# Kernel optimization log

Measured on AMD Instinct MI355X. Metric: run time of the kernel, lower is better.

## Reference

```python
import jax, jax.numpy as jnp
import numpy as np

B, DIM, H, W = 4, 128, 128, 128
NH, DH = 8, 16               # num_heads, dim_head = dim // num_heads
GH_HI, GH_LO = 4, 4          # group_split = [4, 4]
WIN = 8                      # window_size for low-freq avgpool
SCALE = DH ** -0.5


def conv1x1(x, w, b):
    # x: (b,c,h,w), w: (o,c), b: (o,)
    return jnp.einsum('bchw,oc->bohw', x, w) + b[None, :, None, None]


def dwconv3(x, w, b):
    # depthwise 3x3, w: (C,1,3,3) OIHW with feature_group_count=C
    y = jax.lax.conv_general_dilated(x, w, (1, 1), 'SAME',
                                     feature_group_count=x.shape[1],
                                     dimension_numbers=('NCHW', 'OIHW', 'NCHW'))
    return y + b[None, :, None, None]


def setup_inputs() -> dict:
    key = jax.random.key(0)
    ks = jax.random.split(key, 10)
    def rn(k, shape, s=0.05):
        return jax.random.normal(k, shape, jnp.float32) * s
    C3 = 3 * GH_HI * DH            # 192: qkv channels for high-freq branch
    CH = GH_HI * DH                # 64:  high-freq value channels
    CL = GH_LO * DH                # 64:  low-freq q channels
    return {
        'x': jax.random.normal(ks[0], (B, DIM, H, W), jnp.float32),
        'Wqkv': rn(ks[1], (C3, DIM)), 'bqkv': jnp.zeros((C3,), jnp.float32),
        'Wdw': rn(ks[2], (C3, 1, 3, 3)), 'bdw': jnp.zeros((C3,), jnp.float32),
        'Wa1': rn(ks[3], (CH, CH)), 'ba1': jnp.zeros((CH,), jnp.float32),
        'Wa2': rn(ks[4], (CH, CH)), 'ba2': jnp.zeros((CH,), jnp.float32),
        'Wq': rn(ks[5], (CL, DIM)), 'bq': jnp.zeros((CL,), jnp.float32),
        'Wkv': rn(ks[6], (2 * CL, DIM)), 'bkv': jnp.zeros((2 * CL,), jnp.float32),
        'Wproj': rn(ks[7], (DIM, DIM)), 'bproj': jnp.zeros((DIM,), jnp.float32),
    }


def reference(x, Wqkv, bqkv, Wdw, bdw, Wa1, ba1, Wa2, ba2, Wq, bq, Wkv, bkv, Wproj, bproj):
    b = x.shape[0]
    # ---- high-frequency branch: conv qkv -> depthwise mix -> AttnMap(q*k) -> tanh gate * v
    qkv = dwconv3(conv1x1(x, Wqkv, bqkv), Wdw, bdw)          # (b, 3*64, h, w)
    q, k, v = jnp.split(qkv, 3, axis=1)                      # each (b, 64, h, w)
    a = conv1x1(q * k, Wa1, ba1)
    a = a * jax.nn.sigmoid(a)                                # MemoryEfficientSwish
    a = conv1x1(a, Wa2, ba2)
    res_h = jnp.tanh(a * SCALE) * v                          # (b, 64, h, w)
    # ---- low-frequency branch: full-res Q vs avgpooled KV softmax attention
    qg = conv1x1(x, Wq, bq).reshape(b, GH_LO, DH, H * W).transpose(0, 1, 3, 2)  # (b,h,hw,d)
    xp = x.reshape(b, DIM, H // WIN, WIN, W // WIN, WIN).mean((3, 5))           # avgpool 8x8
    hw_p = (H // WIN) * (W // WIN)
    kv = conv1x1(xp, Wkv, bkv).reshape(b, 2, GH_LO, DH, hw_p).transpose(1, 0, 2, 4, 3)
    k2, v2 = kv[0], kv[1]                                     # (b, heads, hw_p, d)
    attn = jax.nn.softmax(SCALE * jnp.einsum('bhnd,bhmd->bhnm', qg, k2), axis=-1)
    res_l = jnp.einsum('bhnm,bhmd->bhnd', attn, v2)           # (b, heads, hw, d)
    res_l = res_l.transpose(0, 1, 3, 2).reshape(b, GH_LO * DH, H, W)
    # ---- concat branches and project
    return conv1x1(jnp.concatenate([res_h, res_l], axis=1), Wproj, bproj)
```

## Files before the change

kernel.cpp:

```cpp
#include <hip/hip_runtime.h>
#include <hip/hip_bf16.h>

typedef __hip_bfloat16 bf16;
typedef short short8v __attribute__((ext_vector_type(8)));
typedef short short4v __attribute__((ext_vector_type(4)));
typedef float floatx4 __attribute__((ext_vector_type(4)));

#define HW 16384

__device__ __forceinline__ float b2f(bf16 v) { return __bfloat162float(v); }
__device__ __forceinline__ bf16 f2b(float v) { return __float2bfloat16(v); }
__device__ __forceinline__ short f2bs(float v) { bf16 h = __float2bfloat16(v); return __builtin_bit_cast(short, h); }
__device__ __forceinline__ float bs2f(short s) { return b2f(__builtin_bit_cast(bf16, s)); }
__device__ __forceinline__ int wuniform(int v) { return __builtin_amdgcn_readfirstlane(v); }

#define OFFB_XP    0u
#define OFFB_K2    524288u
#define OFFB_V2    786432u
#define OFFB_QKVG  (1u << 20)
#define OFFB_RESH  (33u << 20)

__global__ __launch_bounds__(256) void k_pool(const float* __restrict__ x, float* __restrict__ xp,
                                              const float* __restrict__ Wqkv, const float* __restrict__ Wq,
                                              short* __restrict__ wconv)
{
    int idx = blockIdx.x * 256 + threadIdx.x;
    int j = idx & 15, i = (idx >> 4) & 15, bc = idx >> 8;
    const float* src = x + (size_t)bc * HW + (i * 8) * 128 + j * 8;
    float s = 0.f;
    #pragma unroll
    for (int u = 0; u < 8; u++) {
        #pragma unroll
        for (int t = 0; t < 8; t++) s += src[u * 128 + t];
    }
    xp[bc * 256 + i * 16 + j] = s * (1.f / 64.f);

    if (blockIdx.x < 8) {
        int base = blockIdx.x * 4096 + threadIdx.x * 16;
        #pragma unroll
        for (int e = 0; e < 16; e += 4) {
            int k = base + e;
            const float* ws = (k < 24576) ? (Wqkv + k) : (Wq + k - 24576);
            floatx4 wv = *(const floatx4*)ws;
            short4v pk;
            pk[0] = f2bs(wv[0]); pk[1] = f2bs(wv[1]); pk[2] = f2bs(wv[2]); pk[3] = f2bs(wv[3]);
            *(short4v*)&wconv[k] = pk;
        }
    }
}

__global__ __launch_bounds__(256) void k_kv(const float* __restrict__ xp,
                                            const float* __restrict__ Wkv, const float* __restrict__ bkv,
                                            float* __restrict__ k2, float* __restrict__ v2)
{
    __shared__ float w_s[128];
    int o = blockIdx.x & 127, b = blockIdx.x >> 7;
    int m = threadIdx.x;
    if (m < 128) w_s[m] = Wkv[o * 128 + m];
    __syncthreads();
    const float* xb = xp + b * 32768 + m;
    float s0 = 0.f, s1 = 0.f, s2 = 0.f, s3 = 0.f;
    #pragma unroll
    for (int c = 0; c < 128; c += 4) {
        s0 += w_s[c]     * xb[(size_t)(c)     * 256];
        s1 += w_s[c + 1] * xb[(size_t)(c + 1) * 256];
        s2 += w_s[c + 2] * xb[(size_t)(c + 2) * 256];
        s3 += w_s[c + 3] * xb[(size_t)(c + 3) * 256];
    }
    float a = bkv[o] + ((s0 + s1) + (s2 + s3));
    int sb = o >> 6, r = o & 63, gh = r >> 4, dh = r & 15;
    float* dst = sb == 0 ? k2 : v2;
    dst[((b * 4 + gh) * 256 + m) * 16 + dh] = a;
}

__global__ __launch_bounds__(256) void k_conv(const float* __restrict__ x,
                                              const short* __restrict__ wconv,
                                              const float* __restrict__ bqkv, const float* __restrict__ bq,
                                              bf16* __restrict__ qkvg)
{
    __shared__ short a_s[128 * 128];
    __shared__ short b_s[128 * 128];
    __shared__ float bias_s[256];
    int t = threadIdx.x;
    int b = blockIdx.y;
    int px0 = blockIdx.x * 128;

    bias_s[t] = (t < 192) ? bqkv[t] : bq[t - 192];

    int wave = wuniform(t >> 6);
    int lane = t & 63;
    int quad = lane >> 4, l16 = lane & 15;
    int pxs = t & 127, chalf = (t >> 7) * 64;

    {
        const float* xb = x + (size_t)b * 128 * HW + px0 + pxs;
        #pragma unroll
        for (int p = 0; p < 8; p++) {
            int c0 = chalf + p * 8;
            float xv[8];
            #pragma unroll
            for (int jj = 0; jj < 8; jj++) xv[jj] = xb[(size_t)(c0 + jj) * HW];
            short8v pk;
            #pragma unroll
            for (int jj = 0; jj < 8; jj++) pk[jj] = f2bs(xv[jj]);
            *(short8v*)&b_s[((c0 >> 3) * 128 + pxs) * 8] = pk;
        }
    }

    #pragma unroll 1
    for (int my = 0; my < 2; my++) {
        __syncthreads();
        const short* wsrc = wconv + my * 16384;
        #pragma unroll
        for (int i = 0; i < 8; i++) {
            int idx = i * 2048 + t * 8;
            *(short8v*)&a_s[idx] = *(const short8v*)&wsrc[idx];
        }
        __syncthreads();

        floatx4 acc[2][8] = {};
        #pragma unroll
        for (int kk = 0; kk < 4; kk++) {
            short8v a0 = *(const short8v*)&a_s[(wave * 32 + l16) * 128 + kk * 32 + quad * 8];
            short8v a1 = *(const short8v*)&a_s[(wave * 32 + 16 + l16) * 128 + kk * 32 + quad * 8];
            #pragma unroll
            for (int nt = 0; nt < 8; nt++) {
                short8v bv = *(const short8v*)&b_s[((kk * 4 + quad) * 128 + nt * 16 + l16) * 8];
                acc[0][nt] = __builtin_amdgcn_mfma_f32_16x16x32_bf16(a0, bv, acc[0][nt], 0, 0, 0);
                acc[1][nt] = __builtin_amdgcn_mfma_f32_16x16x32_bf16(a1, bv, acc[1][nt], 0, 0, 0);
            }
        }
        #pragma unroll
        for (int m = 0; m < 2; m++) {
            int rowb = wave * 32 + m * 16 + quad * 4;
            #pragma unroll
            for (int nt = 0; nt < 8; nt++) {
                int px = px0 + nt * 16 + l16;
                #pragma unroll
                for (int r = 0; r < 4; r++) {
                    int row = rowb + r;
                    float val = acc[m][nt][r] + bias_s[my * 128 + row];
                    qkvg[((size_t)b * 256 + my * 128 + row) * HW + px] = f2b(val);
                }
            }
        }
    }
}

__global__ __launch_bounds__(256) void k_dw(const bf16* __restrict__ qkvg,
                                            const float* __restrict__ Wdw, const float* __restrict__ bdw,
                                            bf16* __restrict__ p, bf16* __restrict__ v)
{
    int blk = blockIdx.x;
    int bc = blk >> 3;
    int c = bc & 63, b = bc >> 6;
    int g = (blk & 7) * 256 + threadIdx.x;
    int i = g >> 4;
    int j0 = (g & 15) * 8;
    float acc[3][8];
    #pragma unroll
    for (int pl = 0; pl < 3; pl++) {
        float bias = bdw[pl * 64 + c];
        #pragma unroll
        for (int t2 = 0; t2 < 8; t2++) acc[pl][t2] = bias;
    }
    #pragma unroll
    for (int pl = 0; pl < 3; pl++) {
        const bf16* plane = qkvg + (size_t)(b * 256 + pl * 64 + c) * HW;
        const float* w = Wdw + (pl * 64 + c) * 9;
        #pragma unroll
        for (int dy = 0; dy < 3; dy++) {
            int ii = i + dy - 1;
            float e[10];
            if ((unsigned)ii < 128u) {
                const bf16* r = plane + ii * 128 + j0;
                short8v v8 = *(const short8v*)r;
                #pragma unroll
                for (int t2 = 0; t2 < 8; t2++) e[t2 + 1] = bs2f(v8[t2]);
                e[0] = (j0 > 0) ? b2f(r[-1]) : 0.f;
                e[9] = (j0 < 120) ? b2f(r[8]) : 0.f;
            } else {
                #pragma unroll
                for (int t2 = 0; t2 < 10; t2++) e[t2] = 0.f;
            }
            float wa = w[dy * 3], wb = w[dy * 3 + 1], wc = w[dy * 3 + 2];
            #pragma unroll
            for (int t2 = 0; t2 < 8; t2++)
                acc[pl][t2] += wa * e[t2] + wb * e[t2 + 1] + wc * e[t2 + 2];
        }
    }
    short8v pv, vv;
    #pragma unroll
    for (int t2 = 0; t2 < 8; t2++) {
        pv[t2] = f2bs(acc[0][t2] * acc[1][t2]);
        vv[t2] = f2bs(acc[2][t2]);
    }
    size_t off = (size_t)(b * 64 + c) * HW + i * 128 + j0;
    *(short8v*)(p + off) = pv;
    *(short8v*)(v + off) = vv;
}

__global__ __launch_bounds__(256, 6) void k_attn(bf16* __restrict__ qkvg, const float* __restrict__ k2,
                                                 const float* __restrict__ v2)
{
    __shared__ short kt[16 * 64 * 8];
    __shared__ short vt[8 * 64 * 8];
    int t = threadIdx.x;
    int h = blockIdx.y, b = blockIdx.z;
    int px0b = blockIdx.x * 64;
    const float* K = k2 + (size_t)(b * 4 + h) * 4096;
    const float* V = v2 + (size_t)(b * 4 + h) * 4096;
    bf16* Qbase = qkvg + (size_t)(b * 256 + 192 + h * 16) * HW + px0b;

    {
        int mb = t >> 5, kl = t & 31, q = kl >> 3, s = kl & 7;
        int tile = 2 * mb + (s >> 2), row = q * 4 + (s & 3);
        float4 k0 = *(const float4*)(K + t * 16);
        float4 k1 = *(const float4*)(K + t * 16 + 4);
        float4 kx2 = *(const float4*)(K + t * 16 + 8);
        float4 k3 = *(const float4*)(K + t * 16 + 12);
        short8v lo, hi, zz = {};
        lo[0] = f2bs(k0.x); lo[1] = f2bs(k0.y); lo[2] = f2bs(k0.z); lo[3] = f2bs(k0.w);
        lo[4] = f2bs(k1.x); lo[5] = f2bs(k1.y); lo[6] = f2bs(k1.z); lo[7] = f2bs(k1.w);
        hi[0] = f2bs(kx2.x); hi[1] = f2bs(kx2.y); hi[2] = f2bs(kx2.z); hi[3] = f2bs(kx2.w);
        hi[4] = f2bs(k3.x); hi[5] = f2bs(k3.y); hi[6] = f2bs(k3.z); hi[7] = f2bs(k3.w);
        *(short8v*)&kt[(tile * 64 + row) * 8] = lo;
        *(short8v*)&kt[(tile * 64 + 16 + row) * 8] = hi;
        *(short8v*)&kt[(tile * 64 + 32 + row) * 8] = zz;
        *(short8v*)&kt[(tile * 64 + 48 + row) * 8] = zz;
    }
    #pragma unroll
    for (int u = 0; u < 2; u++) {
        int f = t * 2 + u;
        int mb = f >> 6, lane = f & 63, quad = lane >> 4, d = lane & 15;
        short8v pk;
        #pragma unroll
        for (int i = 0; i < 8; i++) pk[i] = f2bs(V[(mb * 32 + quad * 8 + i) * 16 + d]);
        *(short8v*)&vt[f * 8] = pk;
    }

    int wave = wuniform(t >> 6);
    int lane = t & 63;
    int quad = lane >> 4, l16 = lane & 15;
    short8v qf = {};
    if (quad < 2) {
        int px = wave * 16 + l16;
        #pragma unroll
        for (int i = 0; i < 8; i++)
            qf[i] = f2bs(b2f(Qbase[(size_t)(quad * 8 + i) * HW + px]) * 0.36067376022224085f);
    }
    __syncthreads();

    {
        int pxt = wave;
        floatx4 denv = {};
        floatx4 oa = {};
        #pragma unroll
        for (int mb = 0; mb < 8; mb++) {
            short8v kfE = *(const short8v*)&kt[((2 * mb) * 64 + lane) * 8];
            short8v kfO = *(const short8v*)&kt[((2 * mb + 1) * 64 + lane) * 8];
            floatx4 scE = __builtin_amdgcn_mfma_f32_16x16x32_bf16(kfE, qf, (floatx4){0.f, 0.f, 0.f, 0.f}, 0, 0, 0);
            floatx4 scO = __builtin_amdgcn_mfma_f32_16x16x32_bf16(kfO, qf, (floatx4){0.f, 0.f, 0.f, 0.f}, 0, 0, 0);
            floatx4 peE, peO;
            #pragma unroll
            for (int r = 0; r < 4; r++) {
                peE[r] = exp2f(fminf(scE[r], 86.f));
                peO[r] = exp2f(fminf(scO[r], 86.f));
            }
            denv += peE;
            denv += peO;
            short8v pa;
            pa[0] = f2bs(peE[0]); pa[1] = f2bs(peE[1]); pa[2] = f2bs(peE[2]); pa[3] = f2bs(peE[3]);
            pa[4] = f2bs(peO[0]); pa[5] = f2bs(peO[1]); pa[6] = f2bs(peO[2]); pa[7] = f2bs(peO[3]);
            short8v vf = *(const short8v*)&vt[(mb * 64 + lane) * 8];
            oa = __builtin_amdgcn_mfma_f32_16x16x32_bf16(vf, pa, oa, 0, 0, 0);
        }
        float den = (denv[0] + denv[1]) + (denv[2] + denv[3]);
        den += __shfl_xor(den, 16, 64);
        den += __shfl_xor(den, 32, 64);
        float rden = 1.f / den;
        #pragma unroll
        for (int r = 0; r < 4; r++)
            Qbase[(size_t)(quad * 4 + r) * HW + pxt * 16 + l16] = f2b(oa[r] * rden);
    }
}

__global__ __launch_bounds__(256) void k_wcvt(const float* __restrict__ Wproj,
                                              const float* __restrict__ Wa1, const float* __restrict__ Wa2,
                                              short* __restrict__ wdst)
{
    int idx = blockIdx.x * 1024 + threadIdx.x * 4;
    const float* src;
    if (idx < 16384)      src = Wproj + idx;
    else if (idx < 20480) src = Wa1 + (idx - 16384);
    else                  src = Wa2 + (idx - 20480);
    floatx4 wv = *(const floatx4*)src;
    short4v pk;
    pk[0] = f2bs(wv[0]); pk[1] = f2bs(wv[1]); pk[2] = f2bs(wv[2]); pk[3] = f2bs(wv[3]);
    *(short4v*)&wdst[idx] = pk;
}

__global__ __launch_bounds__(256) void k_resh(const bf16* __restrict__ p, const bf16* __restrict__ vhat,
                                              const short* __restrict__ wabf,
                                              const float* __restrict__ ba1, const float* __restrict__ ba2,
                                              bf16* __restrict__ resh)
{
    __shared__ short aw1[64 * 64];
    __shared__ short aw2[64 * 64];
    __shared__ short bp[8 * 128 * 8];
    __shared__ short bs2[8 * 128 * 8];
    __shared__ float b1s[64], b2s[64];
    int t = threadIdx.x;
    int b = blockIdx.y;
    int px0 = blockIdx.x * 128;

    if (t < 64) { b1s[t] = ba1[t]; b2s[t] = ba2[t]; }
    #pragma unroll
    for (int i = 0; i < 2; i++) {
        int idx = i * 2048 + t * 8;
        *(short8v*)&aw1[idx] = *(const short8v*)&wabf[idx];
        *(short8v*)&aw2[idx] = *(const short8v*)&wabf[4096 + idx];
    }
    {
        int pxs = t & 127, chalf = (t >> 7) * 32;
        const short* pb = (const short*)p + (size_t)b * 64 * HW + px0 + pxs;
        #pragma unroll
        for (int pp = 0; pp < 4; pp++) {
            int c0 = chalf + pp * 8;
            short8v pk;
            #pragma unroll
            for (int jj = 0; jj < 8; jj++) pk[jj] = pb[(size_t)(c0 + jj) * HW];
            *(short8v*)&bp[((c0 >> 3) * 128 + pxs) * 8] = pk;
        }
    }
    __syncthreads();

    int wave = wuniform(t >> 6);
    int lane = t & 63;
    int quad = lane >> 4, l16 = lane & 15;
    int k0 = wave * 16 + quad * 4;

    floatx4 acc1[8] = {};
    #pragma unroll
    for (int kk = 0; kk < 2; kk++) {
        short8v af = *(const short8v*)&aw1[(wave * 16 + l16) * 64 + kk * 32 + quad * 8];
        #pragma unroll
        for (int nt = 0; nt < 8; nt++) {
            short8v bf = *(const short8v*)&bp[((kk * 4 + quad) * 128 + nt * 16 + l16) * 8];
            acc1[nt] = __builtin_amdgcn_mfma_f32_16x16x32_bf16(af, bf, acc1[nt], 0, 0, 0);
        }
    }
    #pragma unroll
    for (int nt = 0; nt < 8; nt++) {
        int px = nt * 16 + l16;
        short4v pk;
        #pragma unroll
        for (int r = 0; r < 4; r++) {
            float a = acc1[nt][r] + b1s[k0 + r];
            pk[r] = f2bs(a / (1.f + __expf(-a)));
        }
        *(short4v*)&bs2[((k0 >> 3) * 128 + px) * 8 + (k0 & 7)] = pk;
    }
    __syncthreads();

    floatx4 acc2[8] = {};
    #pragma unroll
    for (int kk = 0; kk < 2; kk++) {
        short8v af = *(const short8v*)&aw2[(wave * 16 + l16) * 64 + kk * 32 + quad * 8];
        #pragma unroll
        for (int nt = 0; nt < 8; nt++) {
            short8v bf = *(const short8v*)&bs2[((kk * 4 + quad) * 128 + nt * 16 + l16) * 8];
            acc2[nt] = __builtin_amdgcn_mfma_f32_16x16x32_bf16(af, bf, acc2[nt], 0, 0, 0);
        }
    }
    #pragma unroll
    for (int nt = 0; nt < 8; nt++) {
        int px = px0 + nt * 16 + l16;
        #pragma unroll
        for (int r = 0; r < 4; r++) {
            int oc = k0 + r;
            float g = tanhf((acc2[nt][r] + b2s[oc]) * 0.25f);
            float vv = b2f(vhat[(size_t)(b * 64 + oc) * HW + px]);
            resh[(size_t)(b * 64 + oc) * HW + px] = f2b(g * vv);
        }
    }
}

__global__ __launch_bounds__(256) void k_proj(const bf16* __restrict__ resh, const bf16* __restrict__ qkvg,
                                              const short* __restrict__ wpbf, const float* __restrict__ bproj,
                                              float* __restrict__ out)
{
    __shared__ short a_s[128 * 128];
    __shared__ short b_s[128 * 128];
    __shared__ float bias_s[128];
    int t = threadIdx.x;
    int b = blockIdx.y;
    int px0 = blockIdx.x * 128;
    const bf16* resl = qkvg + (size_t)(b * 256 + 192) * HW;

    if (t < 128) bias_s[t] = bproj[t];
    #pragma unroll
    for (int i = 0; i < 8; i++) {
        int idx = i * 2048 + t * 8;
        *(short8v*)&a_s[idx] = *(const short8v*)&wpbf[idx];
    }
    {
        int pxs = t & 127, half = t >> 7;
        const short* srcb = half == 0 ? ((const short*)resh + (size_t)b * 64 * HW + px0 + pxs)
                                      : ((const short*)resl + px0 + pxs);
        #pragma unroll
        for (int pp = 0; pp < 8; pp++) {
            int c0 = half * 64 + pp * 8;
            short8v pk;
            #pragma unroll
            for (int jj = 0; jj < 8; jj++) pk[jj] = srcb[(size_t)(pp * 8 + jj) * HW];
            *(short8v*)&b_s[((c0 >> 3) * 128 + pxs) * 8] = pk;
        }
    }
    __syncthreads();

    int wave = wuniform(t >> 6);
    int lane = t & 63;
    int quad = lane >> 4, l16 = lane & 15;
    floatx4 acc[2][8] = {};
    #pragma unroll
    for (int kk = 0; kk < 4; kk++) {
        short8v a0 = *(const short8v*)&a_s[(wave * 32 + l16) * 128 + kk * 32 + quad * 8];
        short8v a1 = *(const short8v*)&a_s[(wave * 32 + 16 + l16) * 128 + kk * 32 + quad * 8];
        #pragma unroll
        for (int nt = 0; nt < 8; nt++) {
            short8v bv = *(const short8v*)&b_s[((kk * 4 + quad) * 128 + nt * 16 + l16) * 8];
            acc[0][nt] = __builtin_amdgcn_mfma_f32_16x16x32_bf16(a0, bv, acc[0][nt], 0, 0, 0);
            acc[1][nt] = __builtin_amdgcn_mfma_f32_16x16x32_bf16(a1, bv, acc[1][nt], 0, 0, 0);
        }
    }
    #pragma unroll
    for (int m = 0; m < 2; m++) {
        int rowb = wave * 32 + m * 16 + quad * 4;
        #pragma unroll
        for (int nt = 0; nt < 8; nt++) {
            int px = px0 + nt * 16 + l16;
            #pragma unroll
            for (int r = 0; r < 4; r++) {
                int row = rowb + r;
                out[((size_t)b * 128 + row) * HW + px] = acc[m][nt][r] + bias_s[row];
            }
        }
    }
}

extern "C" void kernel_launch(void* const* d_in, const int* in_sizes, int n_in,
                              void* d_out, int out_size, void* d_ws, size_t ws_size,
                              hipStream_t stream)
{
    (void)in_sizes; (void)n_in; (void)out_size; (void)ws_size;
    const float* x     = (const float*)d_in[0];
    const float* Wqkv  = (const float*)d_in[1];
    const float* bqkv  = (const float*)d_in[2];
    const float* Wdw   = (const float*)d_in[3];
    const float* bdw   = (const float*)d_in[4];
    const float* Wa1   = (const float*)d_in[5];
    const float* ba1   = (const float*)d_in[6];
    const float* Wa2   = (const float*)d_in[7];
    const float* ba2   = (const float*)d_in[8];
    const float* Wq    = (const float*)d_in[9];
    const float* bq    = (const float*)d_in[10];
    const float* Wkv   = (const float*)d_in[11];
    const float* bkv   = (const float*)d_in[12];
    const float* Wproj = (const float*)d_in[13];
    const float* bproj = (const float*)d_in[14];

    char* wsb = (char*)d_ws;
    float* xp   = (float*)(wsb + OFFB_XP);
    float* k2   = (float*)(wsb + OFFB_K2);
    float* v2   = (float*)(wsb + OFFB_V2);
    bf16*  qkvg = (bf16*)(wsb + OFFB_QKVG);
    bf16*  resh = (bf16*)(wsb + OFFB_RESH);
    short* wconv = (short*)(wsb + OFFB_RESH);
    short* wlate = (short*)(wsb + OFFB_K2);
    bf16*  p    = (bf16*)d_out;
    bf16*  v    = (bf16*)d_out + 4194304;
    float* out  = (float*)d_out;

    k_pool<<<dim3(512), 256, 0, stream>>>(x, xp, Wqkv, Wq, wconv);
    k_kv<<<dim3(512), 256, 0, stream>>>(xp, Wkv, bkv, k2, v2);
    k_conv<<<dim3(128, 4), 256, 0, stream>>>(x, wconv, bqkv, bq, qkvg);
    k_dw<<<dim3(2048), 256, 0, stream>>>(qkvg, Wdw, bdw, p, v);
    k_attn<<<dim3(256, 4, 4), 256, 0, stream>>>(qkvg, k2, v2);
    k_wcvt<<<dim3(24), 256, 0, stream>>>(Wproj, Wa1, Wa2, wlate);
    k_resh<<<dim3(128, 4), 256, 0, stream>>>(p, v, wlate + 16384, ba1, ba2, resh);
    k_proj<<<dim3(128, 4), 256, 0, stream>>>(resh, qkvg, wlate, bproj, out);
}
```

Before: 200.9 us.

## Merge independent kernels into combined launches via block-index branching

Cuts the launch count from eight to four by packing independent stages into one grid each: pointwise QKV conv with avgpool, KV projection with depthwise conv, and low-frequency attention with the high-frequency gating MLP. Block ID picks which stage a block runs. Weight conversion to bf16, previously done by separate kernels, now happens inside each consumer block. The goal is to remove launch gaps and let small stages overlap with large ones, at the cost of repeating the weight conversion in every block and sizing shared memory for the larger branch.

```diff
diff --git a/kernel.cpp b/kernel.cpp
--- a/kernel.cpp
+++ b/kernel.cpp
@@ -20,374 +20,363 @@
 #define OFFB_QKVG  (1u << 20)
 #define OFFB_RESH  (33u << 20)
 
-__global__ __launch_bounds__(256) void k_pool(const float* __restrict__ x, float* __restrict__ xp,
-                                              const float* __restrict__ Wqkv, const float* __restrict__ Wq,
-                                              short* __restrict__ wconv)
+__global__ __launch_bounds__(256) void k_fuseA(const float* __restrict__ x,
+                                               const float* __restrict__ Wqkv, const float* __restrict__ bqkv,
+                                               const float* __restrict__ Wq,  const float* __restrict__ bq,
+                                               bf16* __restrict__ qkvg, float* __restrict__ xp)
 {
-    int idx = blockIdx.x * 256 + threadIdx.x;
-    int j = idx & 15, i = (idx >> 4) & 15, bc = idx >> 8;
-    const float* src = x + (size_t)bc * HW + (i * 8) * 128 + j * 8;
-    float s = 0.f;
-    #pragma unroll
-    for (int u = 0; u < 8; u++) {
-        #pragma unroll
-        for (int t = 0; t < 8; t++) s += src[u * 128 + t];
-    }
-    xp[bc * 256 + i * 16 + j] = s * (1.f / 64.f);
-
-    if (blockIdx.x < 8) {
-        int base = blockIdx.x * 4096 + threadIdx.x * 16;
-        #pragma unroll
-        for (int e = 0; e < 16; e += 4) {
-            int k = base + e;
-            const float* ws = (k < 24576) ? (Wqkv + k) : (Wq + k - 24576);
-            floatx4 wv = *(const floatx4*)ws;
-            short4v pk;
-            pk[0] = f2bs(wv[0]); pk[1] = f2bs(wv[1]); pk[2] = f2bs(wv[2]); pk[3] = f2bs(wv[3]);
-            *(short4v*)&wconv[k] = pk;
-        }
+    __shared__ __align__(16) char smem[66560];
+    int t = threadIdx.x;
+    int bid = blockIdx.x;
+
+    if (bid < 512) {
+        short* a_s = (short*)smem;
+        short* b_s = (short*)(smem + 32768);
+        float* bias_s = (float*)(smem + 65536);
+        int b = bid >> 7;
+        int px0 = (bid & 127) * 128;
+
+        bias_s[t] = (t < 192) ? bqkv[t] : bq[t - 192];
+
+        int wave = wuniform(t >> 6);
+        int lane = t & 63;
+        int quad = lane >> 4, l16 = lane & 15;
+        int pxs = t & 127, chalf = (t >> 7) * 64;
+
+        {
+            const float* xb = x + (size_t)b * 128 * HW + px0 + pxs;
+            #pragma unroll
+            for (int p = 0; p < 8; p++) {
+                int c0 = chalf + p * 8;
+                float xv[8];
+                #pragma unroll
+                for (int jj = 0; jj < 8; jj++) xv[jj] = xb[(size_t)(c0 + jj) * HW];
+                short8v pk;
+                #pragma unroll
+                for (int jj = 0; jj < 8; jj++) pk[jj] = f2bs(xv[jj]);
+                *(short8v*)&b_s[((c0 >> 3) * 128 + pxs) * 8] = pk;
+            }
+        }
+
+        #pragma unroll 1
+        for (int my = 0; my < 2; my++) {
+            __syncthreads();
+            #pragma unroll
+            for (int i = 0; i < 16; i++) {
+                int idx = i * 1024 + t * 4;
+                int row = idx >> 7, col = idx & 127;
+                int oc = my * 128 + row;
+                const float* srcw = (oc < 192) ? (Wqkv + oc * 128 + col) : (Wq + (oc - 192) * 128 + col);
+                floatx4 wv = *(const floatx4*)srcw;
+                short4v pk4;
+                pk4[0] = f2bs(wv[0]); pk4[1] = f2bs(wv[1]); pk4[2] = f2bs(wv[2]); pk4[3] = f2bs(wv[3]);
+                *(short4v*)&a_s[row * 128 + col] = pk4;
+            }
+            __syncthreads();
+
+            floatx4 acc[2][8] = {};
+            #pragma unroll
+            for (int kk = 0; kk < 4; kk++) {
+                short8v a0 = *(const short8v*)&a_s[(wave * 32 + l16) * 128 + kk * 32 + quad * 8];
+                short8v a1 = *(const short8v*)&a_s[(wave * 32 + 16 + l16) * 128 + kk * 32 + quad * 8];
+                #pragma unroll
+                for (int nt = 0; nt < 8; nt++) {
+                    short8v bv = *(const short8v*)&b_s[((kk * 4 + quad) * 128 + nt * 16 + l16) * 8];
+                    acc[0][nt] = __builtin_amdgcn_mfma_f32_16x16x32_bf16(a0, bv, acc[0][nt], 0, 0, 0);
+                    acc[1][nt] = __builtin_amdgcn_mfma_f32_16x16x32_bf16(a1, bv, acc[1][nt], 0, 0, 0);
+                }
+            }
+            #pragma unroll
+            for (int m = 0; m < 2; m++) {
+                int rowb = wave * 32 + m * 16 + quad * 4;
+                #pragma unroll
+                for (int nt = 0; nt < 8; nt++) {
+                    int px = px0 + nt * 16 + l16;
+                    #pragma unroll
+                    for (int r = 0; r < 4; r++) {
+                        int row = rowb + r;
+                        float val = acc[m][nt][r] + bias_s[my * 128 + row];
+                        qkvg[((size_t)b * 256 + my * 128 + row) * HW + px] = f2b(val);
+                    }
+                }
+            }
+        }
+    } else {
+        int idx = (bid - 512) * 256 + t;
+        int j = idx & 15, i = (idx >> 4) & 15, bc = idx >> 8;
+        const float* src = x + (size_t)bc * HW + (i * 8) * 128 + j * 8;
+        float s = 0.f;
+        #pragma unroll
+        for (int u = 0; u < 8; u++) {
+            #pragma unroll
+            for (int t2 = 0; t2 < 8; t2++) s += src[u * 128 + t2];
+        }
+        xp[bc * 256 + i * 16 + j] = s * (1.f / 64.f);
     }
 }
 
-__global__ __launch_bounds__(256) void k_kv(const float* __restrict__ xp,
-                                            const float* __restrict__ Wkv, const float* __restrict__ bkv,
-                                            float* __restrict__ k2, float* __restrict__ v2)
+__global__ __launch_bounds__(256) void k_fuseB(const float* __restrict__ xp,
+                                               const float* __restrict__ Wkv, const float* __restrict__ bkv,
+                                               float* __restrict__ k2, float* __restrict__ v2,
+                                               const bf16* __restrict__ qkvg,
+                                               const float* __restrict__ Wdw, const float* __restrict__ bdw,
+                                               bf16* __restrict__ p, bf16* __restrict__ v)
 {
     __shared__ float w_s[128];
-    int o = blockIdx.x & 127, b = blockIdx.x >> 7;
-    int m = threadIdx.x;
-    if (m < 128) w_s[m] = Wkv[o * 128 + m];
-    __syncthreads();
-    const float* xb = xp + b * 32768 + m;
-    float s0 = 0.f, s1 = 0.f, s2 = 0.f, s3 = 0.f;
-    #pragma unroll
-    for (int c = 0; c < 128; c += 4) {
-        s0 += w_s[c]     * xb[(size_t)(c)     * 256];
-        s1 += w_s[c + 1] * xb[(size_t)(c + 1) * 256];
-        s2 += w_s[c + 2] * xb[(size_t)(c + 2) * 256];
-        s3 += w_s[c + 3] * xb[(size_t)(c + 3) * 256];
-    }
-    float a = bkv[o] + ((s0 + s1) + (s2 + s3));
-    int sb = o >> 6, r = o & 63, gh = r >> 4, dh = r & 15;
-    float* dst = sb == 0 ? k2 : v2;
-    dst[((b * 4 + gh) * 256 + m) * 16 + dh] = a;
+    int t = threadIdx.x;
+    int bid = blockIdx.x;
+
+    if (bid < 512) {
+        int o = bid & 127, b = bid >> 7;
+        int m = t;
+        if (m < 128) w_s[m] = Wkv[o * 128 + m];
+        __syncthreads();
+        const float* xb = xp + b * 32768 + m;
+        float s0 = 0.f, s1 = 0.f, s2 = 0.f, s3 = 0.f;
+        #pragma unroll
+        for (int c = 0; c < 128; c += 4) {
+            s0 += w_s[c]     * xb[(size_t)(c)     * 256];
+            s1 += w_s[c + 1] * xb[(size_t)(c + 1) * 256];
+            s2 += w_s[c + 2] * xb[(size_t)(c + 2) * 256];
+            s3 += w_s[c + 3] * xb[(size_t)(c + 3) * 256];
+        }
+        float a = bkv[o] + ((s0 + s1) + (s2 + s3));
+        int sb = o >> 6, r = o & 63, gh = r >> 4, dh = r & 15;
+        float* dst = sb == 0 ? k2 : v2;
+        dst[((b * 4 + gh) * 256 + m) * 16 + dh] = a;
+    } else {
+        int blk = bid - 512;
+        int bc = blk >> 3;
+        int c = bc & 63, b = bc >> 6;
+        int g = (blk & 7) * 256 + t;
+        int i = g >> 4;
+        int j0 = (g & 15) * 8;
+        float acc[3][8];
+        #pragma unroll
+        for (int pl = 0; pl < 3; pl++) {
+            float bias = bdw[pl * 64 + c];
+            #pragma unroll
+            for (int t2 = 0; t2 < 8; t2++) acc[pl][t2] = bias;
+        }
+        #pragma unroll
+        for (int pl = 0; pl < 3; pl++) {
+            const bf16* plane = qkvg + (size_t)(b * 256 + pl * 64 + c) * HW;
+            const float* w = Wdw + (pl * 64 + c) * 9;
+            #pragma unroll
+            for (int dy = 0; dy < 3; dy++) {
+                int ii = i + dy - 1;
+                float e[10];
+                if ((unsigned)ii < 128u) {
+                    const bf16* r = plane + ii * 128 + j0;
+                    short8v v8 = *(const short8v*)r;
+                    #pragma unroll
+                    for (int t2 = 0; t2 < 8; t2++) e[t2 + 1] = bs2f(v8[t2]);
+                    e[0] = (j0 > 0) ? b2f(r[-1]) : 0.f;
+                    e[9] = (j0 < 120) ? b2f(r[8]) : 0.f;
+                } else {
+                    #pragma unroll
+                    for (int t2 = 0; t2 < 10; t2++) e[t2] = 0.f;
+                }
+                float wa = w[dy * 3], wb = w[dy * 3 + 1], wc = w[dy * 3 + 2];
+                #pragma unroll
+                for (int t2 = 0; t2 < 8; t2++)
+                    acc[pl][t2] += wa * e[t2] + wb * e[t2 + 1] + wc * e[t2 + 2];
+            }
+        }
+        short8v pv, vv;
+        #pragma unroll
+        for (int t2 = 0; t2 < 8; t2++) {
+            pv[t2] = f2bs(acc[0][t2] * acc[1][t2]);
+            vv[t2] = f2bs(acc[2][t2]);
+        }
+        size_t off = (size_t)(b * 64 + c) * HW + i * 128 + j0;
+        *(short8v*)(p + off) = pv;
+        *(short8v*)(v + off) = vv;
+    }
 }
 
-__global__ __launch_bounds__(256) void k_conv(const float* __restrict__ x,
-                                              const short* __restrict__ wconv,
-                                              const float* __restrict__ bqkv, const float* __restrict__ bq,
-                                              bf16* __restrict__ qkvg)
+__global__ __launch_bounds__(256) void k_fuseC(bf16* __restrict__ qkvg,
+                                               const float* __restrict__ k2, const float* __restrict__ v2,
+                                               const bf16* __restrict__ p, const bf16* __restrict__ vhat,
+                                               const float* __restrict__ Wa1, const float* __restrict__ ba1,
+                                               const float* __restrict__ Wa2, const float* __restrict__ ba2,
+                                               bf16* __restrict__ resh)
 {
-    __shared__ short a_s[128 * 128];
-    __shared__ short b_s[128 * 128];
-    __shared__ float bias_s[256];
+    __shared__ __align__(16) char smem[49664];
     int t = threadIdx.x;
-    int b = blockIdx.y;
-    int px0 = blockIdx.x * 128;
-
-    bias_s[t] = (t < 192) ? bqkv[t] : bq[t - 192];
-
-    int wave = wuniform(t >> 6);
-    int lane = t & 63;
-    int quad = lane >> 4, l16 = lane & 15;
-    int pxs = t & 127, chalf = (t >> 7) * 64;
-
-    {
-        const float* xb = x + (size_t)b * 128 * HW + px0 + pxs;
-        #pragma unroll
-        for (int p = 0; p < 8; p++) {
-            int c0 = chalf + p * 8;
-            float xv[8];
-            #pragma unroll
-            for (int jj = 0; jj < 8; jj++) xv[jj] = xb[(size_t)(c0 + jj) * HW];
+    int bid = blockIdx.x;
+
+    if (bid < 512) {
+        short* aw1 = (short*)smem;
+        short* aw2 = (short*)(smem + 8192);
+        short* bp  = (short*)(smem + 16384);
+        short* bs2 = (short*)(smem + 32768);
+        float* b1s = (float*)(smem + 49152);
+        float* b2s = (float*)(smem + 49408);
+        int b = bid >> 7;
+        int px0 = (bid & 127) * 128;
+
+        if (t < 64) { b1s[t] = ba1[t]; b2s[t] = ba2[t]; }
+        #pragma unroll
+        for (int i = 0; i < 4; i++) {
+            int idx = i * 1024 + t * 4;
+            floatx4 w1 = *(const floatx4*)(Wa1 + idx);
+            floatx4 w2 = *(const floatx4*)(Wa2 + idx);
+            short4v p1, p2;
+            #pragma unroll
+            for (int e = 0; e < 4; e++) { p1[e] = f2bs(w1[e]); p2[e] = f2bs(w2[e]); }
+            *(short4v*)&aw1[idx] = p1;
+            *(short4v*)&aw2[idx] = p2;
+        }
+        {
+            int pxs = t & 127, chalf = (t >> 7) * 32;
+            const short* pb = (const short*)p + (size_t)b * 64 * HW + px0 + pxs;
+            #pragma unroll
+            for (int pp = 0; pp < 4; pp++) {
+                int c0 = chalf + pp * 8;
+                short8v pk;
+                #pragma unroll
+                for (int jj = 0; jj < 8; jj++) pk[jj] = pb[(size_t)(c0 + jj) * HW];
+                *(short8v*)&bp[((c0 >> 3) * 128 + pxs) * 8] = pk;
+            }
+        }
+        __syncthreads();
+
+        int wave = wuniform(t >> 6);
+        int lane = t & 63;
+        int quad = lane >> 4, l16 = lane & 15;
+        int k0 = wave * 16 + quad * 4;
+
+        floatx4 acc1[8] = {};
+        #pragma unroll
+        for (int kk = 0; kk < 2; kk++) {
+            short8v af = *(const short8v*)&aw1[(wave * 16 + l16) * 64 + kk * 32 + quad * 8];
+            #pragma unroll
+            for (int nt = 0; nt < 8; nt++) {
+                short8v bf = *(const short8v*)&bp[((kk * 4 + quad) * 128 + nt * 16 + l16) * 8];
+                acc1[nt] = __builtin_amdgcn_mfma_f32_16x16x32_bf16(af, bf, acc1[nt], 0, 0, 0);
+            }
+        }
+        #pragma unroll
+        for (int nt = 0; nt < 8; nt++) {
+            int px = nt * 16 + l16;
+            short4v pk;
+            #pragma unroll
+            for (int r = 0; r < 4; r++) {
+                float a = acc1[nt][r] + b1s[k0 + r];
+                pk[r] = f2bs(a / (1.f + __expf(-a)));
+            }
+            *(short4v*)&bs2[((k0 >> 3) * 128 + px) * 8 + (k0 & 7)] = pk;
+        }
+        __syncthreads();
+
+        floatx4 acc2[8] = {};
+        #pragma unroll
+        for (int kk = 0; kk < 2; kk++) {
+            short8v af = *(const short8v*)&aw2[(wave * 16 + l16) * 64 + kk * 32 + quad * 8];
+            #pragma unroll
+            for (int nt = 0; nt < 8; nt++) {
+                short8v bf = *(const short8v*)&bs2[((kk * 4 + quad) * 128 + nt * 16 + l16) * 8];
+                acc2[nt] = __builtin_amdgcn_mfma_f32_16x16x32_bf16(af, bf, acc2[nt], 0, 0, 0);
+            }
+        }
+        #pragma unroll
+        for (int nt = 0; nt < 8; nt++) {
+            int px = px0 + nt * 16 + l16;
+            #pragma unroll
+            for (int r = 0; r < 4; r++) {
+                int oc = k0 + r;
+                float g = tanhf((acc2[nt][r] + b2s[oc]) * 0.25f);
+                float vv = b2f(vhat[(size_t)(b * 64 + oc) * HW + px]);
+                resh[(size_t)(b * 64 + oc) * HW + px] = f2b(g * vv);
+            }
+        }
+    } else {
+        short* kt = (short*)smem;
+        short* vt = (short*)(smem + 16384);
+        int abid = bid - 512;
+        int h = (abid >> 8) & 3, b = abid >> 10;
+        int px0b = (abid & 255) * 64;
+        const float* K = k2 + (size_t)(b * 4 + h) * 4096;
+        const float* V = v2 + (size_t)(b * 4 + h) * 4096;
+        bf16* Qbase = qkvg + (size_t)(b * 256 + 192 + h * 16) * HW + px0b;
+
+        {
+            int mb = t >> 5, kl = t & 31, q = kl >> 3, s = kl & 7;
+            int tile = 2 * mb + (s >> 2), row = q * 4 + (s & 3);
+            float4 k0 = *(const float4*)(K + t * 16);
+            float4 k1 = *(const float4*)(K + t * 16 + 4);
+            float4 kx2 = *(const float4*)(K + t * 16 + 8);
+            float4 k3 = *(const float4*)(K + t * 16 + 12);
+            short8v lo, hi, zz = {};
+            lo[0] = f2bs(k0.x); lo[1] = f2bs(k0.y); lo[2] = f2bs(k0.z); lo[3] = f2bs(k0.w);
+            lo[4] = f2bs(k1.x); lo[5] = f2bs(k1.y); lo[6] = f2bs(k1.z); lo[7] = f2bs(k1.w);
+            hi[0] = f2bs(kx2.x); hi[1] = f2bs(kx2.y); hi[2] = f2bs(kx2.z); hi[3] = f2bs(kx2.w);
+            hi[4] = f2bs(k3.x); hi[5] = f2bs(k3.y); hi[6] = f2bs(k3.z); hi[7] = f2bs(k3.w);
+            *(short8v*)&kt[(tile * 64 + row) * 8] = lo;
+            *(short8v*)&kt[(tile * 64 + 16 + row) * 8] = hi;
+            *(short8v*)&kt[(tile * 64 + 32 + row) * 8] = zz;
+            *(short8v*)&kt[(tile * 64 + 48 + row) * 8] = zz;
+        }
+        #pragma unroll
+        for (int u = 0; u < 2; u++) {
+            int f = t * 2 + u;
+            int mb = f >> 6, lane = f & 63, quad = lane >> 4, d = lane & 15;
             short8v pk;
             #pragma unroll
-            for (int jj = 0; jj < 8; jj++) pk[jj] = f2bs(xv[jj]);
-            *(short8v*)&b_s[((c0 >> 3) * 128 + pxs) * 8] = pk;
-        }
-    }
-
-    #pragma unroll 1
-    for (int my = 0; my < 2; my++) {
+            for (int i = 0; i < 8; i++) pk[i] = f2bs(V[(mb * 32 + quad * 8 + i) * 16 + d]);
+            *(short8v*)&vt[f * 8] = pk;
+        }
+
+        int wave = wuniform(t >> 6);
+        int lane = t & 63;
+        int quad = lane >> 4, l16 = lane & 15;
+        short8v qf = {};
+        if (quad < 2) {
+            int px = wave * 16 + l16;
+            #pragma unroll
+            for (int i = 0; i < 8; i++)
+                qf[i] = f2bs(b2f(Qbase[(size_t)(quad * 8 + i) * HW + px]) * 0.36067376022224085f);
+        }
         __syncthreads();
-        const short* wsrc = wconv + my * 16384;
-        #pragma unroll
-        for (int i = 0; i < 8; i++) {
-            int idx = i * 2048 + t * 8;
-            *(short8v*)&a_s[idx] = *(const short8v*)&wsrc[idx];
-        }
-        __syncthreads();
-
-        floatx4 acc[2][8] = {};
-        #pragma unroll
-        for (int kk = 0; kk < 4; kk++) {
-            short8v a0 = *(const short8v*)&a_s[(wave * 32 + l16) * 128 + kk * 32 + quad * 8];
-            short8v a1 = *(const short8v*)&a_s[(wave * 32 + 16 + l16) * 128 + kk * 32 + quad * 8];
-            #pragma unroll
-            for (int nt = 0; nt < 8; nt++) {
-                short8v bv = *(const short8v*)&b_s[((kk * 4 + quad) * 128 + nt * 16 + l16) * 8];
-                acc[0][nt] = __builtin_amdgcn_mfma_f32_16x16x32_bf16(a0, bv, acc[0][nt], 0, 0, 0);
-                acc[1][nt] = __builtin_amdgcn_mfma_f32_16x16x32_bf16(a1, bv, acc[1][nt], 0, 0, 0);
-            }
-        }
-        #pragma unroll
-        for (int m = 0; m < 2; m++) {
-            int rowb = wave * 32 + m * 16 + quad * 4;
-            #pragma unroll
-            for (int nt = 0; nt < 8; nt++) {
-                int px = px0 + nt * 16 + l16;
+
+        {
+            int pxt = wave;
+            floatx4 denv = {};
+            floatx4 oa = {};
+            #pragma unroll
+            for (int mb = 0; mb < 8; mb++) {
+                short8v kfE = *(const short8v*)&kt[((2 * mb) * 64 + lane) * 8];
+                short8v kfO = *(const short8v*)&kt[((2 * mb + 1) * 64 + lane) * 8];
+                floatx4 scE = __builtin_amdgcn_mfma_f32_16x16x32_bf16(kfE, qf, (floatx4){0.f, 0.f, 0.f, 0.f}, 0, 0, 0);
+                floatx4 scO = __builtin_amdgcn_mfma_f32_16x16x32_bf16(kfO, qf, (floatx4){0.f, 0.f, 0.f, 0.f}, 0, 0, 0);
+                floatx4 peE, peO;
                 #pragma unroll
                 for (int r = 0; r < 4; r++) {
-                    int row = rowb + r;
-                    float val = acc[m][nt][r] + bias_s[my * 128 + row];
-                    qkvg[((size_t)b * 256 + my * 128 + row) * HW + px] = f2b(val);
+                    peE[r] = exp2f(fminf(scE[r], 86.f));
+                    peO[r] = exp2f(fminf(scO[r], 86.f));
                 }
-            }
+                denv += peE;
+                denv += peO;
+                short8v pa;
+                pa[0] = f2bs(peE[0]); pa[1] = f2bs(peE[1]); pa[2] = f2bs(peE[2]); pa[3] = f2bs(peE[3]);
+                pa[4] = f2bs(peO[0]); pa[5] = f2bs(peO[1]); pa[6] = f2bs(peO[2]); pa[7] = f2bs(peO[3]);
+                short8v vf = *(const short8v*)&vt[(mb * 64 + lane) * 8];
+                oa = __builtin_amdgcn_mfma_f32_16x16x32_bf16(vf, pa, oa, 0, 0, 0);
+            }
+            float den = (denv[0] + denv[1]) + (denv[2] + denv[3]);
+            den += __shfl_xor(den, 16, 64);
+            den += __shfl_xor(den, 32, 64);
+            float rden = 1.f / den;
+            #pragma unroll
+            for (int r = 0; r < 4; r++)
+                Qbase[(size_t)(quad * 4 + r) * HW + pxt * 16 + l16] = f2b(oa[r] * rden);
         }
     }
 }
 
-__global__ __launch_bounds__(256) void k_dw(const bf16* __restrict__ qkvg,
-                                            const float* __restrict__ Wdw, const float* __restrict__ bdw,
-                                            bf16* __restrict__ p, bf16* __restrict__ v)
-{
-    int blk = blockIdx.x;
-    int bc = blk >> 3;
-    int c = bc & 63, b = bc >> 6;
-    int g = (blk & 7) * 256 + threadIdx.x;
-    int i = g >> 4;
-    int j0 = (g & 15) * 8;
-    float acc[3][8];
-    #pragma unroll
-    for (int pl = 0; pl < 3; pl++) {
-        float bias = bdw[pl * 64 + c];
-        #pragma unroll
-        for (int t2 = 0; t2 < 8; t2++) acc[pl][t2] = bias;
-    }
-    #pragma unroll
-    for (int pl = 0; pl < 3; pl++) {
-        const bf16* plane = qkvg + (size_t)(b * 256 + pl * 64 + c) * HW;
-        const float* w = Wdw + (pl * 64 + c) * 9;
-        #pragma unroll
-        for (int dy = 0; dy < 3; dy++) {
-            int ii = i + dy - 1;
-            float e[10];
-            if ((unsigned)ii < 128u) {
-                const bf16* r = plane + ii * 128 + j0;
-                short8v v8 = *(const short8v*)r;
-                #pragma unroll
-                for (int t2 = 0; t2 < 8; t2++) e[t2 + 1] = bs2f(v8[t2]);
-                e[0] = (j0 > 0) ? b2f(r[-1]) : 0.f;
-                e[9] = (j0 < 120) ? b2f(r[8]) : 0.f;
-            } else {
-                #pragma unroll
-                for (int t2 = 0; t2 < 10; t2++) e[t2] = 0.f;
-            }
-            float wa = w[dy * 3], wb = w[dy * 3 + 1], wc = w[dy * 3 + 2];
-            #pragma unroll
-            for (int t2 = 0; t2 < 8; t2++)
-                acc[pl][t2] += wa * e[t2] + wb * e[t2 + 1] + wc * e[t2 + 2];
-        }
-    }
-    short8v pv, vv;
-    #pragma unroll
-    for (int t2 = 0; t2 < 8; t2++) {
-        pv[t2] = f2bs(acc[0][t2] * acc[1][t2]);
-        vv[t2] = f2bs(acc[2][t2]);
-    }
-    size_t off = (size_t)(b * 64 + c) * HW + i * 128 + j0;
-    *(short8v*)(p + off) = pv;
-    *(short8v*)(v + off) = vv;
-}
-
-__global__ __launch_bounds__(256, 6) void k_attn(bf16* __restrict__ qkvg, const float* __restrict__ k2,
-                                                 const float* __restrict__ v2)
-{
-    __shared__ short kt[16 * 64 * 8];
-    __shared__ short vt[8 * 64 * 8];
-    int t = threadIdx.x;
-    int h = blockIdx.y, b = blockIdx.z;
-    int px0b = blockIdx.x * 64;
-    const float* K = k2 + (size_t)(b * 4 + h) * 4096;
-    const float* V = v2 + (size_t)(b * 4 + h) * 4096;
-    bf16* Qbase = qkvg + (size_t)(b * 256 + 192 + h * 16) * HW + px0b;
-
-    {
-        int mb = t >> 5, kl = t & 31, q = kl >> 3, s = kl & 7;
-        int tile = 2 * mb + (s >> 2), row = q * 4 + (s & 3);
-        float4 k0 = *(const float4*)(K + t * 16);
-        float4 k1 = *(const float4*)(K + t * 16 + 4);
-        float4 kx2 = *(const float4*)(K + t * 16 + 8);
-        float4 k3 = *(const float4*)(K + t * 16 + 12);
-        short8v lo, hi, zz = {};
-        lo[0] = f2bs(k0.x); lo[1] = f2bs(k0.y); lo[2] = f2bs(k0.z); lo[3] = f2bs(k0.w);
-        lo[4] = f2bs(k1.x); lo[5] = f2bs(k1.y); lo[6] = f2bs(k1.z); lo[7] = f2bs(k1.w);
-        hi[0] = f2bs(kx2.x); hi[1] = f2bs(kx2.y); hi[2] = f2bs(kx2.z); hi[3] = f2bs(kx2.w);
-        hi[4] = f2bs(k3.x); hi[5] = f2bs(k3.y); hi[6] = f2bs(k3.z); hi[7] = f2bs(k3.w);
-        *(short8v*)&kt[(tile * 64 + row) * 8] = lo;
-        *(short8v*)&kt[(tile * 64 + 16 + row) * 8] = hi;
-        *(short8v*)&kt[(tile * 64 + 32 + row) * 8] = zz;
-        *(short8v*)&kt[(tile * 64 + 48 + row) * 8] = zz;
-    }
-    #pragma unroll
-    for (int u = 0; u < 2; u++) {
-        int f = t * 2 + u;
-        int mb = f >> 6, lane = f & 63, quad = lane >> 4, d = lane & 15;
-        short8v pk;
-        #pragma unroll
-        for (int i = 0; i < 8; i++) pk[i] = f2bs(V[(mb * 32 + quad * 8 + i) * 16 + d]);
-        *(short8v*)&vt[f * 8] = pk;
-    }
-
-    int wave = wuniform(t >> 6);
-    int lane = t & 63;
-    int quad = lane >> 4, l16 = lane & 15;
-    short8v qf = {};
-    if (quad < 2) {
-        int px = wave * 16 + l16;
-        #pragma unroll
-        for (int i = 0; i < 8; i++)
-            qf[i] = f2bs(b2f(Qbase[(size_t)(quad * 8 + i) * HW + px]) * 0.36067376022224085f);
-    }
-    __syncthreads();
-
-    {
-        int pxt = wave;
-        floatx4 denv = {};
-        floatx4 oa = {};
-        #pragma unroll
-        for (int mb = 0; mb < 8; mb++) {
-            short8v kfE = *(const short8v*)&kt[((2 * mb) * 64 + lane) * 8];
-            short8v kfO = *(const short8v*)&kt[((2 * mb + 1) * 64 + lane) * 8];
-            floatx4 scE = __builtin_amdgcn_mfma_f32_16x16x32_bf16(kfE, qf, (floatx4){0.f, 0.f, 0.f, 0.f}, 0, 0, 0);
-            floatx4 scO = __builtin_amdgcn_mfma_f32_16x16x32_bf16(kfO, qf, (floatx4){0.f, 0.f, 0.f, 0.f}, 0, 0, 0);
-            floatx4 peE, peO;
-            #pragma unroll
-            for (int r = 0; r < 4; r++) {
-                peE[r] = exp2f(fminf(scE[r], 86.f));
-                peO[r] = exp2f(fminf(scO[r], 86.f));
-            }
-            denv += peE;
-            denv += peO;
-            short8v pa;
-            pa[0] = f2bs(peE[0]); pa[1] = f2bs(peE[1]); pa[2] = f2bs(peE[2]); pa[3] = f2bs(peE[3]);
-            pa[4] = f2bs(peO[0]); pa[5] = f2bs(peO[1]); pa[6] = f2bs(peO[2]); pa[7] = f2bs(peO[3]);
-            short8v vf = *(const short8v*)&vt[(mb * 64 + lane) * 8];
-            oa = __builtin_amdgcn_mfma_f32_16x16x32_bf16(vf, pa, oa, 0, 0, 0);
-        }
-        float den = (denv[0] + denv[1]) + (denv[2] + denv[3]);
-        den += __shfl_xor(den, 16, 64);
-        den += __shfl_xor(den, 32, 64);
-        float rden = 1.f / den;
-        #pragma unroll
-        for (int r = 0; r < 4; r++)
-            Qbase[(size_t)(quad * 4 + r) * HW + pxt * 16 + l16] = f2b(oa[r] * rden);
-    }
-}
-
-__global__ __launch_bounds__(256) void k_wcvt(const float* __restrict__ Wproj,
-                                              const float* __restrict__ Wa1, const float* __restrict__ Wa2,
-                                              short* __restrict__ wdst)
-{
-    int idx = blockIdx.x * 1024 + threadIdx.x * 4;
-    const float* src;
-    if (idx < 16384)      src = Wproj + idx;
-    else if (idx < 20480) src = Wa1 + (idx - 16384);
-    else                  src = Wa2 + (idx - 20480);
-    floatx4 wv = *(const floatx4*)src;
-    short4v pk;
-    pk[0] = f2bs(wv[0]); pk[1] = f2bs(wv[1]); pk[2] = f2bs(wv[2]); pk[3] = f2bs(wv[3]);
-    *(short4v*)&wdst[idx] = pk;
-}
-
-__global__ __launch_bounds__(256) void k_resh(const bf16* __restrict__ p, const bf16* __restrict__ vhat,
-                                              const short* __restrict__ wabf,
-                                              const float* __restrict__ ba1, const float* __restrict__ ba2,
-                                              bf16* __restrict__ resh)
-{
-    __shared__ short aw1[64 * 64];
-    __shared__ short aw2[64 * 64];
-    __shared__ short bp[8 * 128 * 8];
-    __shared__ short bs2[8 * 128 * 8];
-    __shared__ float b1s[64], b2s[64];
-    int t = threadIdx.x;
-    int b = blockIdx.y;
-    int px0 = blockIdx.x * 128;
-
-    if (t < 64) { b1s[t] = ba1[t]; b2s[t] = ba2[t]; }
-    #pragma unroll
-    for (int i = 0; i < 2; i++) {
-        int idx = i * 2048 + t * 8;
-        *(short8v*)&aw1[idx] = *(const short8v*)&wabf[idx];
-        *(short8v*)&aw2[idx] = *(const short8v*)&wabf[4096 + idx];
-    }
-    {
-        int pxs = t & 127, chalf = (t >> 7) * 32;
-        const short* pb = (const short*)p + (size_t)b * 64 * HW + px0 + pxs;
-        #pragma unroll
-        for (int pp = 0; pp < 4; pp++) {
-            int c0 = chalf + pp * 8;
-            short8v pk;
-            #pragma unroll
-            for (int jj = 0; jj < 8; jj++) pk[jj] = pb[(size_t)(c0 + jj) * HW];
-            *(short8v*)&bp[((c0 >> 3) * 128 + pxs) * 8] = pk;
-        }
-    }
-    __syncthreads();
-
-    int wave = wuniform(t >> 6);
-    int lane = t & 63;
-    int quad = lane >> 4, l16 = lane & 15;
-    int k0 = wave * 16 + quad * 4;
-
-    floatx4 acc1[8] = {};
-    #pragma unroll
-    for (int kk = 0; kk < 2; kk++) {
-        short8v af = *(const short8v*)&aw1[(wave * 16 + l16) * 64 + kk * 32 + quad * 8];
-        #pragma unroll
-        for (int nt = 0; nt < 8; nt++) {
-            short8v bf = *(const short8v*)&bp[((kk * 4 + quad) * 128 + nt * 16 + l16) * 8];
-            acc1[nt] = __builtin_amdgcn_mfma_f32_16x16x32_bf16(af, bf, acc1[nt], 0, 0, 0);
-        }
-    }
-    #pragma unroll
-    for (int nt = 0; nt < 8; nt++) {
-        int px = nt * 16 + l16;
-        short4v pk;
-        #pragma unroll
-        for (int r = 0; r < 4; r++) {
-            float a = acc1[nt][r] + b1s[k0 + r];
-            pk[r] = f2bs(a / (1.f + __expf(-a)));
-        }
-        *(short4v*)&bs2[((k0 >> 3) * 128 + px) * 8 + (k0 & 7)] = pk;
-    }
-    __syncthreads();
-
-    floatx4 acc2[8] = {};
-    #pragma unroll
-    for (int kk = 0; kk < 2; kk++) {
-        short8v af = *(const short8v*)&aw2[(wave * 16 + l16) * 64 + kk * 32 + quad * 8];
-        #pragma unroll
-        for (int nt = 0; nt < 8; nt++) {
-            short8v bf = *(const short8v*)&bs2[((kk * 4 + quad) * 128 + nt * 16 + l16) * 8];
-            acc2[nt] = __builtin_amdgcn_mfma_f32_16x16x32_bf16(af, bf, acc2[nt], 0, 0, 0);
-        }
-    }
-    #pragma unroll
-    for (int nt = 0; nt < 8; nt++) {
-        int px = px0 + nt * 16 + l16;
-        #pragma unroll
-        for (int r = 0; r < 4; r++) {
-            int oc = k0 + r;
-            float g = tanhf((acc2[nt][r] + b2s[oc]) * 0.25f);
-            float vv = b2f(vhat[(size_t)(b * 64 + oc) * HW + px]);
-            resh[(size_t)(b * 64 + oc) * HW + px] = f2b(g * vv);
-        }
-    }
-}
-
 __global__ __launch_bounds__(256) void k_proj(const bf16* __restrict__ resh, const bf16* __restrict__ qkvg,
-                                              const short* __restrict__ wpbf, const float* __restrict__ bproj,
+                                              const float* __restrict__ Wproj, const float* __restrict__ bproj,
                                               float* __restrict__ out)
 {
     __shared__ short a_s[128 * 128];
@@ -400,9 +389,12 @@
 
     if (t < 128) bias_s[t] = bproj[t];
     #pragma unroll
-    for (int i = 0; i < 8; i++) {
-        int idx = i * 2048 + t * 8;
-        *(short8v*)&a_s[idx] = *(const short8v*)&wpbf[idx];
+    for (int i = 0; i < 16; i++) {
+        int idx = i * 1024 + t * 4;
+        floatx4 wv = *(const floatx4*)(Wproj + idx);
+        short4v pk;
+        pk[0] = f2bs(wv[0]); pk[1] = f2bs(wv[1]); pk[2] = f2bs(wv[2]); pk[3] = f2bs(wv[3]);
+        *(short4v*)&a_s[idx] = pk;
     }
     {
         int pxs = t & 127, half = t >> 7;
@@ -476,18 +468,12 @@
     float* v2   = (float*)(wsb + OFFB_V2);
     bf16*  qkvg = (bf16*)(wsb + OFFB_QKVG);
     bf16*  resh = (bf16*)(wsb + OFFB_RESH);
-    short* wconv = (short*)(wsb + OFFB_RESH);
-    short* wlate = (short*)(wsb + OFFB_K2);
     bf16*  p    = (bf16*)d_out;
     bf16*  v    = (bf16*)d_out + 4194304;
     float* out  = (float*)d_out;
 
-    k_pool<<<dim3(512), 256, 0, stream>>>(x, xp, Wqkv, Wq, wconv);
-    k_kv<<<dim3(512), 256, 0, stream>>>(xp, Wkv, bkv, k2, v2);
-    k_conv<<<dim3(128, 4), 256, 0, stream>>>(x, wconv, bqkv, bq, qkvg);
-    k_dw<<<dim3(2048), 256, 0, stream>>>(qkvg, Wdw, bdw, p, v);
-    k_attn<<<dim3(256, 4, 4), 256, 0, stream>>>(qkvg, k2, v2);
-    k_wcvt<<<dim3(24), 256, 0, stream>>>(Wproj, Wa1, Wa2, wlate);
-    k_resh<<<dim3(128, 4), 256, 0, stream>>>(p, v, wlate + 16384, ba1, ba2, resh);
-    k_proj<<<dim3(128, 4), 256, 0, stream>>>(resh, qkvg, wlate, bproj, out);
+    k_fuseA<<<dim3(1024), 256, 0, stream>>>(x, Wqkv, bqkv, Wq, bq, qkvg, xp);
+    k_fuseB<<<dim3(2560), 256, 0, stream>>>(xp, Wkv, bkv, k2, v2, qkvg, Wdw, bdw, p, v);
+    k_fuseC<<<dim3(4608), 256, 0, stream>>>(qkvg, k2, v2, p, v, Wa1, ba1, Wa2, ba2, resh);
+    k_proj<<<dim3(128, 4), 256, 0, stream>>>(resh, qkvg, Wproj, bproj, out);
 }
```

After: 193.3 us. -3.8%, faster.
